# Kernel tuning notes

Hardware: AMD Instinct MI355X
Metric: run time of the kernel (lower is better)

The kernel has to match this reference:

```python
import jax, jax.numpy as jnp
import numpy as np

W_DIM = 512
FREQ = 1024
CH = 512
OUT_CH = 512
SIZE = 64
SR = 64.0
BW = 2.0
MAX_BW = BW * 8.0
B = 16
K = 3


def setup_inputs() -> dict:
    key = jax.random.key(0)
    ks = jax.random.split(key, 10)
    w = jax.random.normal(ks[0], (B, W_DIM), dtype=jnp.float32)
    # SynthesisInput buffers: random unit-direction freqs scaled by uniform radius in [0, max_bw)
    f = jax.random.normal(ks[1], (FREQ, 2), dtype=jnp.float32)
    f = f / jnp.linalg.norm(f, axis=1, keepdims=True)
    freqs = f * (jax.random.uniform(ks[2], (FREQ, 1), dtype=jnp.float32) * MAX_BW)
    phases = jax.random.uniform(ks[3], (FREQ,), dtype=jnp.float32) - 0.5
    input_weight = jax.random.normal(ks[4], (CH, FREQ), dtype=jnp.float32)
    # affine: FullyConnectedLayer(w_dim, 4, weight_init=0, bias_init=[1,0,0,0])
    affine_w = jnp.zeros((4, W_DIM), dtype=jnp.float32)
    affine_b = jnp.array([1.0, 0.0, 0.0, 0.0], dtype=jnp.float32)
    # per-layer style affine (w -> in_channels), bias_init=1 (StyleGAN convention)
    style_w = jax.random.normal(ks[5], (CH, W_DIM), dtype=jnp.float32)
    style_b = jnp.ones((CH,), dtype=jnp.float32)
    conv_w = jax.random.normal(ks[6], (OUT_CH, CH, K, K), dtype=jnp.float32)
    conv_b = jnp.zeros((OUT_CH,), dtype=jnp.float32)
    return {"w": w, "affine_w": affine_w, "affine_b": affine_b, "freqs": freqs,
            "phases": phases, "input_weight": input_weight, "style_w": style_w,
            "style_b": style_b, "conv_w": conv_w, "conv_b": conv_b}


def _fc(x, weight, bias):
    # FullyConnectedLayer: weight_gain = 1/sqrt(in_features)
    gain = 1.0 / np.sqrt(weight.shape[1])
    return x @ (weight * gain).T + bias


def _synthesis_input(w, affine_w, affine_b, freqs, phases, input_weight):
    t = _fc(w, affine_w, affine_b)                                  # [B,4]
    t = t / jnp.linalg.norm(t[:, :2], axis=1, keepdims=True)
    c, s, tx, ty = t[:, 0], t[:, 1], t[:, 2], t[:, 3]
    # m = m_r @ m_t (only the 2x3 top block matters)
    rot = jnp.stack([jnp.stack([c, -s], -1), jnp.stack([s, c], -1)], 1)  # [B,2,2]
    trans = jnp.stack([-tx, -ty], -1)                               # [B,2]
    shift = jnp.einsum('bij,bj->bi', rot, trans)                    # [B,2]
    phases_b = phases[None, :] + jnp.einsum('fi,bi->bf', freqs, shift)
    freqs_b = jnp.einsum('fi,bij->bfj', freqs, rot)                 # [B,F,2]
    amp = jnp.clip(1.0 - (jnp.linalg.norm(freqs_b, axis=2) - BW) / (SR / 2.0 - BW), 0.0, 1.0)
    # affine_grid(theta=diag(0.5*size/sr)=0.5, align_corners=False)
    theta00 = 0.5 * SIZE / SR
    xs = ((jnp.arange(SIZE, dtype=jnp.float32) + 0.5) / SIZE * 2.0 - 1.0) * theta00
    ys = ((jnp.arange(SIZE, dtype=jnp.float32) + 0.5) / SIZE * 2.0 - 1.0) * theta00
    gx, gy = jnp.meshgrid(xs, ys)                                   # [H,W]
    grid = jnp.stack([gx, gy], axis=-1)                             # [H,W,2]
    x = jnp.einsum('hwi,bfi->bhwf', grid, freqs_b) + phases_b[:, None, None, :]
    x = jnp.sin(x * (2.0 * np.pi)) * amp[:, None, None, :]
    effect_freq = jnp.sum((jnp.linalg.norm(freqs, axis=-1) < BW).astype(jnp.float32))
    x = jnp.einsum('bhwf,cf->bchw', x, input_weight / jnp.sqrt(effect_freq))
    return x                                                        # [B,CH,H,W]


def _modulated_conv2d(x, weight, s, padding=1):
    # demodulate: pre-normalize w and s
    w_hat = weight * jax.lax.rsqrt(jnp.mean(jnp.square(weight), axis=(1, 2, 3), keepdims=True))
    s_hat = s * jax.lax.rsqrt(jnp.mean(jnp.square(s)))
    # dcoefs[b,o] = rsqrt(sum_ikl (w[o,i,k,l]*s[b,i])^2 + eps)
    dcoefs = jax.lax.rsqrt(jnp.einsum('oikl,bi->bo', jnp.square(w_hat), jnp.square(s_hat)) + 1e-8)
    # grouped-per-sample conv == scale input channels by s, conv with base w, scale out by dcoefs
    x = x * s_hat[:, :, None, None]
    y = jax.lax.conv_general_dilated(x, w_hat, window_strides=(1, 1),
                                     padding=[(padding, padding), (padding, padding)],
                                     dimension_numbers=('NCHW', 'OIHW', 'NCHW'))
    return y * dcoefs[:, :, None, None]


def reference(w, affine_w, affine_b, freqs, phases, input_weight, style_w, style_b, conv_w, conv_b):
    x = _synthesis_input(w, affine_w, affine_b, freqs, phases, input_weight)
    s = _fc(w, style_w, style_b)                                    # [B,CH]
    y = _modulated_conv2d(x, conv_w, s, padding=K // 2)
    y = y + conv_b[None, :, None, None]
    y = jnp.where(y >= 0, y, 0.2 * y) * np.sqrt(2.0)                # lrelu + gain (bias_act)
    y = jnp.clip(y, -256.0, 256.0)                                  # conv_clamp
    return y
```

## Files before the change

kernel.cpp:

```cpp
#include <hip/hip_runtime.h>

typedef __attribute__((ext_vector_type(4))) float f32x4;
typedef __attribute__((ext_vector_type(8))) __bf16 bf16x8;

__device__ __forceinline__ unsigned short f2bf(float f) {
  unsigned int u = __builtin_bit_cast(unsigned int, f);
  return (unsigned short)((u + 0x7FFFu + ((u >> 16) & 1u)) >> 16);
}

__device__ __forceinline__ float sin2pi(float x) {
#if __has_builtin(__builtin_amdgcn_sinf) && __has_builtin(__builtin_amdgcn_fractf)
  return __builtin_amdgcn_sinf(__builtin_amdgcn_fractf(x));
#else
  return __sinf(x * 6.283185307179586f);
#endif
}

__device__ __forceinline__ void gll16(const void* g, void* l) {
  __builtin_amdgcn_global_load_lds(
      (const __attribute__((address_space(1))) void*)g,
      (__attribute__((address_space(3))) void*)l, 16, 0, 0);
}

template <int W>
__device__ __forceinline__ void vmwait() {
  if constexpr (W == 0) asm volatile("s_waitcnt vmcnt(0)" ::: "memory");
  else if constexpr (W == 2) asm volatile("s_waitcnt vmcnt(2)" ::: "memory");
  else if constexpr (W == 4) asm volatile("s_waitcnt vmcnt(4)" ::: "memory");
  else if constexpr (W == 6) asm volatile("s_waitcnt vmcnt(6)" ::: "memory");
  else if constexpr (W == 8) asm volatile("s_waitcnt vmcnt(8)" ::: "memory");
}

#define CFENCE() asm volatile("" ::: "memory")

__global__ void fused_prep_k(const float* __restrict__ w, const float* __restrict__ affine_w,
                             const float* __restrict__ affine_b, const float* __restrict__ freqs,
                             const float* __restrict__ phases, const float* __restrict__ style_w,
                             const float* __restrict__ style_b, const float* __restrict__ conv_w,
                             const float* __restrict__ iw,
                             float4* __restrict__ freq_data, float* __restrict__ scal,
                             float* __restrict__ s_out, float* __restrict__ wsumT,
                             unsigned short* __restrict__ bt_conv,
                             unsigned short* __restrict__ iw_bf,
                             unsigned short* __restrict__ xmp) {
  const int bid = blockIdx.x, tid = threadIdx.x;
  if (bid < 1040) {
    int idx = bid * 256 + tid;
    int chunk = idx & 63;
    int t = idx >> 6;
    int p = t % 260;
    int b = t / 260;
    int h, wq;
    if (p < 66) { h = 0; wq = p; }
    else if (p < 132) { h = 65; wq = p - 66; }
    else if (p < 196) { h = p - 131; wq = 0; }
    else { h = p - 195; wq = 65; }
    uint4 z; z.x = 0; z.y = 0; z.z = 0; z.w = 0;
    *(uint4*)&xmp[(((size_t)b * 66 + h) * 66 + wq) * 512 + chunk * 8] = z;
  } else if (bid < 1056) {
    const int b = bid - 1040;
    const int wv = tid >> 6, lane = tid & 63;
    __shared__ float tdot[4];
    __shared__ float par[4];
    __shared__ float scnt;
    float sum = 0.f;
    for (int i = lane; i < 512; i += 64) sum += w[b * 512 + i] * affine_w[wv * 512 + i];
#pragma unroll
    for (int o = 32; o > 0; o >>= 1) sum += __shfl_down(sum, o);
    if (lane == 0) tdot[wv] = sum;
    if (tid == 0) scnt = 0.f;
    __syncthreads();
    if (tid == 0) {
      const float gain = 0.04419417382415922f;
      float t0 = tdot[0] * gain + affine_b[0];
      float t1 = tdot[1] * gain + affine_b[1];
      float t2 = tdot[2] * gain + affine_b[2];
      float t3 = tdot[3] * gain + affine_b[3];
      float inv = 1.f / sqrtf(t0 * t0 + t1 * t1);
      float c = t0 * inv, s = t1 * inv, tx = t2 * inv, ty = t3 * inv;
      par[0] = c; par[1] = s;
      par[2] = -c * tx + s * ty;
      par[3] = -s * tx - c * ty;
    }
    __syncthreads();
    const float c = par[0], s = par[1], sh0 = par[2], sh1 = par[3];
    float cnt = 0.f;
    for (int f = tid; f < 1024; f += 256) {
      float fx = freqs[2 * f], fy = freqs[2 * f + 1];
      float fb0 = fx * c + fy * s;
      float fb1 = fy * c - fx * s;
      float ph = phases[f] + fx * sh0 + fy * sh1;
      float nb = sqrtf(fb0 * fb0 + fb1 * fb1);
      float amp = fminf(fmaxf(1.f - (nb - 2.f) * (1.f / 30.f), 0.f), 1.f);
      float4 v; v.x = fb0; v.y = fb1; v.z = ph; v.w = amp;
      freq_data[(b << 10) + f] = v;
      if (sqrtf(fx * fx + fy * fy) < 2.f) cnt += 1.f;
    }
    if (b == 0) {
      atomicAdd(&scnt, cnt);
      __syncthreads();
      if (tid == 0) scal[0] = 1.f / sqrtf(scnt);
    }
  } else if (bid < 1184) {
    int gt = (bid - 1056) * 256 + tid;
    int idx = gt >> 2, part = gt & 3;
    int b = idx >> 9, c = idx & 511;
    const float4* wr = (const float4*)(w + b * 512) + part * 32;
    const float4* sr = (const float4*)(style_w + (size_t)c * 512) + part * 32;
    float sum = 0.f;
#pragma unroll 4
    for (int i = 0; i < 32; ++i) {
      float4 a = wr[i], q = sr[i];
      sum += a.x * q.x + a.y * q.y + a.z * q.z + a.w * q.w;
    }
    sum += __shfl_xor(sum, 1);
    sum += __shfl_xor(sum, 2);
    if (part == 0) s_out[idx] = sum * 0.04419417382415922f + style_b[c];
  } else if (bid < 1696) {
    const int o = bid - 1184;
    __shared__ float red[256];
    float sum = 0.f;
    for (int i = tid; i < 4608; i += 256) { float v = conv_w[o * 4608 + i]; sum += v * v; }
    red[tid] = sum;
    __syncthreads();
    for (int off = 128; off > 0; off >>= 1) {
      if (tid < off) red[tid] += red[tid + off];
      __syncthreads();
    }
    const float rn = rsqrtf(red[0] * (1.f / 4608.f));
    for (int i = tid; i < 512; i += 256) {
      float sq = 0.f;
#pragma unroll
      for (int kl = 0; kl < 9; ++kl) {
        float v = conv_w[(o * 512 + i) * 9 + kl];
        sq += v * v;
        bt_conv[o * 4608 + kl * 512 + i] = f2bf(v * rn);
      }
      wsumT[i * 512 + o] = sq * rn * rn;
    }
  } else {
    int i = (bid - 1696) * 256 + tid;
    iw_bf[i] = f2bf(iw[i]);
  }
}

__global__ void shat_dcoef_k(const float* __restrict__ s, const float* __restrict__ wsumT,
                             float* __restrict__ s_hat, float* __restrict__ dcoefs) {
  const int b = blockIdx.x >> 3, og = blockIdx.x & 7, tid = threadIdx.x;
  __shared__ float red[256];
  __shared__ float sh2[512];
  __shared__ float red2[256];
  float sum = 0.f;
  for (int i = tid; i < 8192; i += 256) { float v = s[i]; sum += v * v; }
  red[tid] = sum;
  __syncthreads();
  for (int off = 128; off > 0; off >>= 1) {
    if (tid < off) red[tid] += red[tid + off];
    __syncthreads();
  }
  const float inv_rms = rsqrtf(red[0] * (1.f / 8192.f));
  for (int c = tid; c < 512; c += 256) {
    float sh = s[b * 512 + c] * inv_rms;
    if (og == 0) s_hat[b * 512 + c] = sh;
    sh2[c] = sh * sh;
  }
  __syncthreads();
  const int o = (og << 6) + (tid & 63);
  const int ic = tid >> 6;
  float acc = 0.f;
  for (int i = ic * 128; i < ic * 128 + 128; ++i) acc += wsumT[i * 512 + o] * sh2[i];
  red2[tid] = acc;
  __syncthreads();
  if (tid < 64) {
    float a = red2[tid] + red2[tid + 64] + red2[tid + 128] + red2[tid + 192];
    dcoefs[b * 512 + o] = rsqrtf(a + 1e-8f);
  }
}

__device__ __forceinline__ void sy_sgB(char* lB, const unsigned short* iw, int d,
                                       int rb, int kt, int lane, int lsw) {
  const unsigned short* src = iw + (size_t)(rb + (lane >> 3)) * 1024 + (kt << 6) + lsw;
  gll16(src, lB + d * 65536 + rb * 128);
}

__global__ __launch_bounds__(512, 2) void synth_gemm4_k(
    const float4* __restrict__ freq_data, const unsigned short* __restrict__ iw_bf,
    const float* __restrict__ s_hat, const float* __restrict__ scal,
    unsigned short* __restrict__ xmp) {
  extern __shared__ char sl[];
  char* lA = sl;
  char* lB = sl + 16384;
  const int bid = blockIdx.x;
  const int wg = (bid & 7) * 64 + (bid >> 3);
  const int m0 = wg << 7;
  const int b = m0 >> 12;
  const int hbase = (m0 >> 6) & 63;
  const int tid = threadIdx.x, lane = tid & 63, wv = tid >> 6;
  const int wm = (wv >> 2) << 6;
  const int wn = (wv & 3) << 7;
  const int g = tid & 31;
  const int r0 = (tid >> 5) << 3;
  const int lsw = (((lane & 7) ^ (lane >> 3)) << 3);
  const int aswz = (((lane >> 4) << 4)) ^ ((lane & 7) << 4);
  const char* pA = lA + (size_t)(wm + (lane & 15)) * 128;
  const int browB = wn + (lane & 15);
  f32x4 acc[4][8];
#pragma unroll
  for (int mi = 0; mi < 4; ++mi)
#pragma unroll
    for (int ni = 0; ni < 8; ++ni) { f32x4 z = {0.f, 0.f, 0.f, 0.f}; acc[mi][ni] = z; }
  const float gy0 = (hbase + 0.5f) * 0.015625f - 0.5f;
  const float gy1 = (hbase + 1.5f) * 0.015625f - 0.5f;

#pragma unroll
  for (int ig = 0; ig < 8; ++ig) sy_sgB(lB, iw_bf, 0, wv * 64 + ig * 8, 0, lane, lsw);
  vmwait<0>();
  __builtin_amdgcn_s_barrier();
  CFENCE();

  for (int kt = 0; kt < 16; ++kt) {
    if (kt < 15) {
#pragma unroll
      for (int ig = 0; ig < 8; ++ig)
        sy_sgB(lB, iw_bf, (kt + 1) & 1, wv * 64 + ig * 8, kt + 1, lane, lsw);
    }
    const float4* fdp = freq_data + (b << 10) + (kt << 6) + (g << 1);
    float4 fd0 = fdp[0], fd1 = fdp[1];
#pragma unroll
    for (int j = 0; j < 8; ++j) {
      const int r = r0 + j;
      const float gx = ((r & 63) + 0.5f) * 0.015625f - 0.5f;
      const float gy = (r >> 6) ? gy1 : gy0;
      ushort2 u;
      u.x = f2bf(sin2pi(gx * fd0.x + gy * fd0.y + fd0.z) * fd0.w);
      u.y = f2bf(sin2pi(gx * fd1.x + gy * fd1.y + fd1.z) * fd1.w);
      *(ushort2*)(lA + r * 128 + ((g << 2) ^ ((r & 7) << 4))) = u;
    }
    asm volatile("s_waitcnt lgkmcnt(0)" ::: "memory");
    if (kt < 15) vmwait<8>(); else vmwait<0>();
    __builtin_amdgcn_s_barrier();
    CFENCE();
    __builtin_amdgcn_sched_barrier(0);

    const char* pB = lB + ((kt & 1) << 16) + (size_t)browB * 128;
#pragma unroll
    for (int ks = 0; ks < 2; ++ks) {
      const int ao = aswz ^ (ks << 6);
      bf16x8 af[4], bq[8];
#pragma unroll
      for (int mi = 0; mi < 4; ++mi) af[mi] = *(const bf16x8*)(pA + mi * 2048 + ao);
#pragma unroll
      for (int ni = 0; ni < 8; ++ni) bq[ni] = *(const bf16x8*)(pB + ni * 2048 + ao);
      __builtin_amdgcn_s_setprio(1);
#pragma unroll
      for (int mi = 0; mi < 4; ++mi)
#pragma unroll
        for (int ni = 0; ni < 8; ++ni)
          acc[mi][ni] = __builtin_amdgcn_mfma_f32_16x16x32_bf16(af[mi], bq[ni], acc[mi][ni], 0, 0, 0);
      __builtin_amdgcn_s_setprio(0);
    }
    CFENCE();
    __builtin_amdgcn_s_barrier();
    CFENCE();
  }

  const float inv_eff = scal[0];
  const int c_lo = lane & 15, r_hi = (lane >> 4) << 2;
  unsigned short* lT = (unsigned short*)sl;
#pragma unroll
  for (int ni = 0; ni < 8; ++ni) {
    const int cc = wn + (ni << 4) + c_lo;
    const float sc = s_hat[b * 512 + cc] * inv_eff;
#pragma unroll
    for (int mi = 0; mi < 4; ++mi) {
#pragma unroll
      for (int j = 0; j < 4; ++j) {
        const int rr = wm + (mi << 4) + r_hi + j;
        lT[rr * 520 + cc] = f2bf(acc[mi][ni][j] * sc);
      }
    }
  }
  asm volatile("s_waitcnt lgkmcnt(0)" ::: "memory");
  __builtin_amdgcn_s_barrier();
  CFENCE();
#pragma unroll
  for (int it = 0; it < 16; ++it) {
    const int chunk = it * 512 + tid;
    const int row = chunk >> 6;
    const int co = (chunk & 63) << 3;
    uint4 v = *(const uint4*)&lT[row * 520 + co];
    const int hp = hbase + (row >> 6) + 1;
    const int wp = (row & 63) + 1;
    *(uint4*)&xmp[(((size_t)b * 66 + hp) * 66 + wp) * 512 + co] = v;
  }
}

__device__ __forceinline__ float epi_act(float a, float dco, float cb) {
  float y = a * dco + cb;
  y = (y >= 0.f ? y : 0.2f * y) * 1.4142135623730951f;
  return fminf(fmaxf(y, -256.f), 256.f);
}

struct ConvCtx {
  const unsigned short* xmp;
  const unsigned short* bt;
  int n0, hb, b_img, lane;
  int lsw;
  int gB_rb0;
  int gA_lo;
  int gA_up;
};

__device__ __forceinline__ void tile_geom(int t, int& dh, int& dw, int& kc, int& koff) {
  const int kc8 = t / 9;
  const int off = t - 9 * kc8;
  dh = off / 3;
  dw = off - 3 * dh;
  kc = kc8 << 6;
  koff = off * 512 + kc;
}

__device__ __forceinline__ void sgA(char* lds, const ConvCtx& c, int d, int rb,
                                    int dh, int dw, int kc) {
  const int r = rb + (c.lane >> 3);
  const int h = c.hb + (r >> 6) + dh;
  const int w = (r & 63) + dw;
  const unsigned short* src = c.xmp + (((size_t)c.b_img * 66 + h) * 66 + w) * 512 + kc + c.lsw;
  gll16(src, lds + d * 32768 + rb * 128);
}

__device__ __forceinline__ void sgB(char* lds, const ConvCtx& c, int d, int rb, int koff) {
  const int row = c.n0 + rb + (c.lane >> 3);
  const unsigned short* src = c.bt + (size_t)row * 4608 + koff + c.lsw;
  gll16(src, lds + 65536 + d * 32768 + rb * 128);
}

template <bool STG>
__device__ __forceinline__ void conv_tile1(char* lds, const ConvCtx& c, f32x4 (&acc)[8][4],
                                           const char* pA, const char* pB, int aswz0, int t) {
  int dh1, dw1, kc1, koff1;
  tile_geom(t + 1, dh1, dw1, kc1, koff1);
  const int D = t & 1, Dn = D ^ 1;
  const int db = D << 15;
  const int a0 = aswz0, a1 = aswz0 ^ 64;

  vmwait<0>();
  __builtin_amdgcn_s_barrier();
  CFENCE();
  __builtin_amdgcn_sched_barrier(0);

  bf16x8 bq[4], af[4];
#pragma unroll
  for (int ni = 0; ni < 4; ++ni) bq[ni] = *(const bf16x8*)(pB + db + ni * 2048 + a0);
#pragma unroll
  for (int i = 0; i < 4; ++i) af[i] = *(const bf16x8*)(pA + db + i * 2048 + a0);
  if (STG) {
    sgB(lds, c, Dn, c.gB_rb0, koff1);      sgB(lds, c, Dn, c.gB_rb0 + 8, koff1);
    sgB(lds, c, Dn, c.gB_rb0 + 16, koff1); sgB(lds, c, Dn, c.gB_rb0 + 24, koff1);
  }
  __builtin_amdgcn_s_setprio(1);
#pragma unroll
  for (int i = 0; i < 4; ++i)
#pragma unroll
    for (int ni = 0; ni < 4; ++ni)
      acc[i][ni] = __builtin_amdgcn_mfma_f32_16x16x32_bf16(af[i], bq[ni], acc[i][ni], 0, 0, 0);
  __builtin_amdgcn_s_setprio(0);
#pragma unroll
  for (int i = 0; i < 4; ++i) af[i] = *(const bf16x8*)(pA + db + (4 + i) * 2048 + a0);
  if (STG) {
    sgA(lds, c, Dn, c.gA_up, dh1, dw1, kc1); sgA(lds, c, Dn, c.gA_up + 8, dh1, dw1, kc1);
    sgA(lds, c, Dn, c.gA_lo, dh1, dw1, kc1); sgA(lds, c, Dn, c.gA_lo + 8, dh1, dw1, kc1);
  }
  __builtin_amdgcn_s_setprio(1);
#pragma unroll
  for (int i = 0; i < 4; ++i)
#pragma unroll
    for (int ni = 0; ni < 4; ++ni)
      acc[4 + i][ni] = __builtin_amdgcn_mfma_f32_16x16x32_bf16(af[i], bq[ni], acc[4 + i][ni], 0, 0, 0);
  __builtin_amdgcn_s_setprio(0);
#pragma unroll
  for (int ni = 0; ni < 4; ++ni) bq[ni] = *(const bf16x8*)(pB + db + ni * 2048 + a1);
#pragma unroll
  for (int i = 0; i < 4; ++i) af[i] = *(const bf16x8*)(pA + db + i * 2048 + a1);
  __builtin_amdgcn_s_setprio(1);
#pragma unroll
  for (int i = 0; i < 4; ++i)
#pragma unroll
    for (int ni = 0; ni < 4; ++ni)
      acc[i][ni] = __builtin_amdgcn_mfma_f32_16x16x32_bf16(af[i], bq[ni], acc[i][ni], 0, 0, 0);
  __builtin_amdgcn_s_setprio(0);
#pragma unroll
  for (int i = 0; i < 4; ++i) af[i] = *(const bf16x8*)(pA + db + (4 + i) * 2048 + a1);
  __builtin_amdgcn_s_setprio(1);
#pragma unroll
  for (int i = 0; i < 4; ++i)
#pragma unroll
    for (int ni = 0; ni < 4; ++ni)
      acc[4 + i][ni] = __builtin_amdgcn_mfma_f32_16x16x32_bf16(af[i], bq[ni], acc[4 + i][ni], 0, 0, 0);
  __builtin_amdgcn_s_setprio(0);
  CFENCE();
}

__global__ __launch_bounds__(512, 2) void conv_gemm8_k(
    const unsigned short* __restrict__ xmp, const unsigned short* __restrict__ bt_conv,
    const float* __restrict__ dcoefs, const float* __restrict__ conv_b,
    float* __restrict__ out) {
  extern __shared__ char lds[];
  const int tid = threadIdx.x, lane = tid & 63, wv = tid >> 6;
  const int bid = blockIdx.x;
  const int wg = (bid & 7) * 64 + (bid >> 3);
  const int mt = wg >> 1, nt = wg & 1;
  const int m0 = mt << 8, n0 = nt << 8;
  const int b_img = m0 >> 12;
  const int hb = (m0 >> 6) & 63;
  const int wm = (wv >> 2) << 7, wn = (wv & 3) << 6;

  ConvCtx c;
  c.xmp = xmp; c.bt = bt_conv;
  c.n0 = n0; c.hb = hb; c.b_img = b_img; c.lane = lane;
  c.lsw = (((lane & 7) ^ (lane >> 3)) << 3);
  c.gB_rb0 = (((wv & 3) >> 1) << 7) + (((wv & 1) | ((wv >> 2) << 1)) << 5);
  c.gA_lo = wm + ((wv & 3) << 4);
  c.gA_up = c.gA_lo + 64;

  const char* pA = lds + (size_t)(wm + (lane & 15)) * 128;
  const char* pB = lds + 65536 + (size_t)(wn + (lane & 15)) * 128;
  const int aswz0 = (((lane >> 4) << 4)) ^ ((lane & 7) << 4);

  f32x4 acc[8][4];
#pragma unroll
  for (int mi = 0; mi < 8; ++mi)
#pragma unroll
    for (int ni = 0; ni < 4; ++ni) { f32x4 z = {0.f, 0.f, 0.f, 0.f}; acc[mi][ni] = z; }

  sgB(lds, c, 0, c.gB_rb0, 0);       sgB(lds, c, 0, c.gB_rb0 + 8, 0);
  sgB(lds, c, 0, c.gB_rb0 + 16, 0);  sgB(lds, c, 0, c.gB_rb0 + 24, 0);
  sgA(lds, c, 0, c.gA_up, 0, 0, 0);  sgA(lds, c, 0, c.gA_up + 8, 0, 0, 0);
  sgA(lds, c, 0, c.gA_lo, 0, 0, 0);  sgA(lds, c, 0, c.gA_lo + 8, 0, 0, 0);

  for (int t = 0; t < 71; ++t) conv_tile1<true>(lds, c, acc, pA, pB, aswz0, t);
  conv_tile1<false>(lds, c, acc, pA, pB, aswz0, 71);

  const int c_lo = lane & 15, r_hi = (lane >> 4) << 2;
#pragma unroll
  for (int ni = 0; ni < 4; ++ni) {
    const int oo = n0 + wn + (ni << 4) + c_lo;
    const float dco = dcoefs[b_img * 512 + oo];
    const float cb = conv_b[oo];
#pragma unroll
    for (int mi = 0; mi < 8; ++mi) {
      const int rr = wm + (mi << 4) + r_hi;
      const int hh = hb + (rr >> 6);
      const int w0 = rr & 63;
      float4 v;
      v.x = epi_act(acc[mi][ni][0], dco, cb);
      v.y = epi_act(acc[mi][ni][1], dco, cb);
      v.z = epi_act(acc[mi][ni][2], dco, cb);
      v.w = epi_act(acc[mi][ni][3], dco, cb);
      *(float4*)&out[(((size_t)b_img * 512 + oo) * 64 + hh) * 64 + w0] = v;
    }
  }
}

extern "C" void kernel_launch(void* const* d_in, const int* in_sizes, int n_in,
                              void* d_out, int out_size, void* d_ws, size_t ws_size,
                              hipStream_t stream) {
  (void)in_sizes; (void)n_in; (void)out_size;
  const float* w        = (const float*)d_in[0];
  const float* affine_w = (const float*)d_in[1];
  const float* affine_b = (const float*)d_in[2];
  const float* freqs    = (const float*)d_in[3];
  const float* phases   = (const float*)d_in[4];
  const float* input_weight = (const float*)d_in[5];
  const float* style_w  = (const float*)d_in[6];
  const float* style_b  = (const float*)d_in[7];
  const float* conv_w   = (const float*)d_in[8];
  const float* conv_b   = (const float*)d_in[9];
  float* out = (float*)d_out;

  char* p = (char*)d_ws;
  float4* freq_data = (float4*)p;               p += (size_t)16 * 1024 * 16;
  float* scal = (float*)p;                      p += 256;
  float* s_buf = (float*)p;                     p += 8192 * 4;
  float* s_hat = (float*)p;                     p += 8192 * 4;
  float* wsumT = (float*)p;                     p += (size_t)512 * 512 * 4;
  float* dcoefs = (float*)p;                    p += 8192 * 4;
  unsigned short* iw_bf = (unsigned short*)p;   p += (size_t)512 * 1024 * 2;
  unsigned short* bt_conv = (unsigned short*)p; p += (size_t)512 * 4608 * 2;
  unsigned short* xmp = (unsigned short*)p;     p += (size_t)16 * 66 * 66 * 512 * 2;
  if (ws_size < (size_t)(p - (char*)d_ws)) return;

  (void)hipFuncSetAttribute((const void*)conv_gemm8_k,
                            hipFuncAttributeMaxDynamicSharedMemorySize, 131072);
  (void)hipFuncSetAttribute((const void*)synth_gemm4_k,
                            hipFuncAttributeMaxDynamicSharedMemorySize, 147456);

  fused_prep_k<<<3744, 256, 0, stream>>>(w, affine_w, affine_b, freqs, phases,
                                         style_w, style_b, conv_w, input_weight,
                                         freq_data, scal, s_buf, wsumT, bt_conv,
                                         iw_bf, xmp);
  shat_dcoef_k<<<128, 256, 0, stream>>>(s_buf, wsumT, s_hat, dcoefs);
  synth_gemm4_k<<<512, 512, 147456, stream>>>(freq_data, iw_bf, s_hat, scal, xmp);
  conv_gemm8_k<<<512, 512, 131072, stream>>>(xmp, bt_conv, dcoefs, conv_b, out);
}
```

Before: 392.8 us.

## Double-buffer synthesized A tile and overlap sine generation with MFMA

The synthesis GEMM now double-buffers the on-the-fly sinusoid A tile in LDS. The next k-tile's features are computed after the current tile's MFMAs, and B prefetch is issued after the barrier, so each iteration needs one barrier instead of two. This is meant to hide the sine ALU work behind matrix math. In exchange it uses more LDS per block (160 KB versus 144 KB), which could limit occupancy, and it waits for all outstanding vector memory before each barrier.

```diff
diff --git a/kernel.cpp b/kernel.cpp
--- a/kernel.cpp
+++ b/kernel.cpp
@@ -183,13 +183,13 @@
   gll16(src, lB + d * 65536 + rb * 128);
 }
 
-__global__ __launch_bounds__(512, 2) void synth_gemm4_k(
+__global__ __launch_bounds__(512, 2) void synth_gemm5_k(
     const float4* __restrict__ freq_data, const unsigned short* __restrict__ iw_bf,
     const float* __restrict__ s_hat, const float* __restrict__ scal,
     unsigned short* __restrict__ xmp) {
   extern __shared__ char sl[];
   char* lA = sl;
-  char* lB = sl + 16384;
+  char* lB = sl + 32768;
   const int bid = blockIdx.x;
   const int wg = (bid & 7) * 64 + (bid >> 3);
   const int m0 = wg << 7;
@@ -202,7 +202,7 @@
   const int r0 = (tid >> 5) << 3;
   const int lsw = (((lane & 7) ^ (lane >> 3)) << 3);
   const int aswz = (((lane >> 4) << 4)) ^ ((lane & 7) << 4);
-  const char* pA = lA + (size_t)(wm + (lane & 15)) * 128;
+  const int rowA = (wm + (lane & 15)) * 128;
   const int browB = wn + (lane & 15);
   f32x4 acc[4][8];
 #pragma unroll
@@ -214,17 +214,8 @@
 
 #pragma unroll
   for (int ig = 0; ig < 8; ++ig) sy_sgB(lB, iw_bf, 0, wv * 64 + ig * 8, 0, lane, lsw);
-  vmwait<0>();
-  __builtin_amdgcn_s_barrier();
-  CFENCE();
-
-  for (int kt = 0; kt < 16; ++kt) {
-    if (kt < 15) {
-#pragma unroll
-      for (int ig = 0; ig < 8; ++ig)
-        sy_sgB(lB, iw_bf, (kt + 1) & 1, wv * 64 + ig * 8, kt + 1, lane, lsw);
-    }
-    const float4* fdp = freq_data + (b << 10) + (kt << 6) + (g << 1);
+  {
+    const float4* fdp = freq_data + (b << 10) + (g << 1);
     float4 fd0 = fdp[0], fd1 = fdp[1];
 #pragma unroll
     for (int j = 0; j < 8; ++j) {
@@ -236,13 +227,23 @@
       u.y = f2bf(sin2pi(gx * fd1.x + gy * fd1.y + fd1.z) * fd1.w);
       *(ushort2*)(lA + r * 128 + ((g << 2) ^ ((r & 7) << 4))) = u;
     }
+  }
+
+  for (int kt = 0; kt < 16; ++kt) {
+    const int d = kt & 1, dn = d ^ 1;
     asm volatile("s_waitcnt lgkmcnt(0)" ::: "memory");
-    if (kt < 15) vmwait<8>(); else vmwait<0>();
+    vmwait<0>();
     __builtin_amdgcn_s_barrier();
     CFENCE();
     __builtin_amdgcn_sched_barrier(0);
 
-    const char* pB = lB + ((kt & 1) << 16) + (size_t)browB * 128;
+    if (kt < 15) {
+#pragma unroll
+      for (int ig = 0; ig < 8; ++ig)
+        sy_sgB(lB, iw_bf, dn, wv * 64 + ig * 8, kt + 1, lane, lsw);
+    }
+    const char* pA = lA + d * 16384 + rowA;
+    const char* pB = lB + d * 65536 + (size_t)browB * 128;
 #pragma unroll
     for (int ks = 0; ks < 2; ++ks) {
       const int ao = aswz ^ (ks << 6);
@@ -259,10 +260,25 @@
           acc[mi][ni] = __builtin_amdgcn_mfma_f32_16x16x32_bf16(af[mi], bq[ni], acc[mi][ni], 0, 0, 0);
       __builtin_amdgcn_s_setprio(0);
     }
+    if (kt < 15) {
+      const float4* fdp = freq_data + (b << 10) + ((kt + 1) << 6) + (g << 1);
+      float4 fd0 = fdp[0], fd1 = fdp[1];
+#pragma unroll
+      for (int j = 0; j < 8; ++j) {
+        const int r = r0 + j;
+        const float gx = ((r & 63) + 0.5f) * 0.015625f - 0.5f;
+        const float gy = (r >> 6) ? gy1 : gy0;
+        ushort2 u;
+        u.x = f2bf(sin2pi(gx * fd0.x + gy * fd0.y + fd0.z) * fd0.w);
+        u.y = f2bf(sin2pi(gx * fd1.x + gy * fd1.y + fd1.z) * fd1.w);
+        *(ushort2*)(lA + dn * 16384 + r * 128 + ((g << 2) ^ ((r & 7) << 4))) = u;
+      }
+    }
     CFENCE();
-    __builtin_amdgcn_s_barrier();
-    CFENCE();
-  }
+  }
+  CFENCE();
+  __builtin_amdgcn_s_barrier();
+  CFENCE();
 
   const float inv_eff = scal[0];
   const int c_lo = lane & 15, r_hi = (lane >> 4) << 2;
@@ -492,14 +508,14 @@
 
   (void)hipFuncSetAttribute((const void*)conv_gemm8_k,
                             hipFuncAttributeMaxDynamicSharedMemorySize, 131072);
-  (void)hipFuncSetAttribute((const void*)synth_gemm4_k,
-                            hipFuncAttributeMaxDynamicSharedMemorySize, 147456);
+  (void)hipFuncSetAttribute((const void*)synth_gemm5_k,
+                            hipFuncAttributeMaxDynamicSharedMemorySize, 163840);
 
   fused_prep_k<<<3744, 256, 0, stream>>>(w, affine_w, affine_b, freqs, phases,
                                          style_w, style_b, conv_w, input_weight,
                                          freq_data, scal, s_buf, wsumT, bt_conv,
                                          iw_bf, xmp);
   shat_dcoef_k<<<128, 256, 0, stream>>>(s_buf, wsumT, s_hat, dcoefs);
-  synth_gemm4_k<<<512, 512, 147456, stream>>>(freq_data, iw_bf, s_hat, scal, xmp);
+  synth_gemm5_k<<<512, 512, 163840, stream>>>(freq_data, iw_bf, s_hat, scal, xmp);
   conv_gemm8_k<<<512, 512, 131072, stream>>>(xmp, bt_conv, dcoefs, conv_b, out);
 }
```

Result: faster. 377.3 us (-3.9%).
